# Kernel optimization log

Hardware: AMD Instinct MI355X
Metric: run time of the kernel (lower is better)

The kernel has to match this reference:

```python
import jax, jax.numpy as jnp
import numpy as np

B = 4096        # batch_size
D = 256         # feature_dim
N = 9000000     # dataset size (state buffer length)
G = 100         # num_groups
ALPHA = 0.5     # alpha_weight
GAMMA = 0.8
RHO = 8.0
LAM = 1.0       # lambada
ETA_P = 0.01
EPS = 1e-14
CLIP = 5.0


def setup_inputs() -> dict:
    key = jax.random.key(0)
    k = jax.random.split(key, 6)
    zis = jax.random.normal(k[0], (B, D), jnp.float32)
    zjs = jax.random.normal(k[1], (B, D), jnp.float32)
    # per-sample learned temperatures, small positive values
    taus_I = 0.01 + 0.2 * jax.random.uniform(k[2], (N,), jnp.float32)
    taus_T = 0.01 + 0.2 * jax.random.uniform(k[3], (N,), jnp.float32)
    group_info_I = jax.random.randint(k[4], (N,), 0, G, dtype=jnp.int32)
    group_info_T = jax.random.randint(k[5], (N,), 0, G, dtype=jnp.int32)
    ids = jnp.arange(B, dtype=jnp.int32)  # unique sample indices
    zeros_N = jnp.zeros((N,), jnp.float32)
    return {
        "zis": zis, "zjs": zjs,
        "s_I": zeros_N, "s_T": zeros_N, "b_I": zeros_N, "b_T": zeros_N,
        "z_I": jnp.zeros((G,), jnp.float32), "z_T": jnp.zeros((G,), jnp.float32),
        "p_I": jnp.ones((G,), jnp.float32) / G, "p_T": jnp.ones((G,), jnp.float32) / G,
        "taus_I": taus_I, "taus_T": taus_T,
        "ids": ids, "group_info_I": group_info_I, "group_info_T": group_info_T,
    }


def _l2norm(x):
    return x / jnp.maximum(jnp.linalg.norm(x, axis=1, keepdims=True), 1e-12)


def reference(zis, zjs, s_I, s_T, b_I, b_T, z_I, z_T, p_I, p_T,
              taus_I, taus_T, ids, group_info_I, group_info_T):
    zis = _l2norm(zis)
    zjs = _l2norm(zjs)
    sim = zis @ zjs.T                                   # [B, B]
    diag = jnp.diagonal(sim)                            # [B]
    mask_neg = 1.0 - jnp.eye(B, dtype=sim.dtype)
    image_diffs = sim - diag[:, None]
    text_diffs = sim - diag[None, :]

    tau_I = taus_I[ids]                                 # [B]
    tau_T = taus_T[ids]
    idt = jax.lax.stop_gradient(image_diffs / tau_I[:, None])
    tdt = jax.lax.stop_gradient(text_diffs / tau_T[None, :])

    # running max state (numerically-stable exp)
    old_b_I = b_I[ids]
    b_I_new = jnp.maximum(jnp.max(idt, axis=1), old_b_I)    # [B]
    old_b_T = b_T[ids]
    b_T_new = jnp.maximum(jnp.max(tdt, axis=0), old_b_T)    # [B]
    b_I = b_I.at[ids].set(b_I_new)
    b_T = b_T.at[ids].set(b_T_new)

    exp_I = jnp.exp(idt - b_I_new[:, None]) * mask_neg
    exp_T = jnp.exp(tdt - b_T_new[None, :]) * mask_neg
    g_I = jnp.sum(exp_I, axis=1)                         # [B]
    g_T = jnp.sum(exp_T, axis=0)                         # [B]

    # EMA of softmax denominators with max-rescaling
    s_I_new = (1.0 - GAMMA) * s_I[ids] * jnp.exp(old_b_I - b_I_new) + GAMMA * g_I
    s_T_new = (1.0 - GAMMA) * s_T[ids] * jnp.exp(old_b_T - b_T_new) + GAMMA * g_T
    s_I = s_I.at[ids].set(s_I_new)
    s_T = s_T.at[ids].set(s_T_new)
    s_I_c = jnp.maximum(s_I_new, EPS)
    s_T_c = jnp.maximum(s_T_new, EPS)

    w_I = exp_I / s_I_c[:, None]
    w_T = exp_T / s_T_c[None, :]

    gid_I = group_info_I[ids]                            # [B]
    gid_T = group_info_T[ids]
    gw_I = G * p_I[gid_I]                                # [B]
    gw_T = G * p_T[gid_T]

    image_loss = jnp.sum(w_I * gw_I[:, None] * image_diffs, axis=1)   # [B]
    text_loss = jnp.sum(w_T * gw_T[None, :] * text_diffs, axis=0)     # [B]
    total_loss = ALPHA * image_loss.mean() + (1.0 - ALPHA) * text_loss.mean()

    # per-group adversarial weight update
    F_I = tau_I * (jnp.log(s_I_c) + b_I_new + RHO)       # [B]
    F_T = tau_T * (jnp.log(s_T_c) + b_T_new + RHO)
    ones_b = jnp.ones((B,), sim.dtype)
    cnt_I = jnp.maximum(jax.ops.segment_sum(ones_b, gid_I, num_segments=G), 1.0)
    cnt_T = jnp.maximum(jax.ops.segment_sum(ones_b, gid_T, num_segments=G), 1.0)
    grad_p_I = jax.ops.segment_sum(F_I, gid_I, num_segments=G) / cnt_I
    grad_p_T = jax.ops.segment_sum(F_T, gid_T, num_segments=G) / cnt_T

    z_I = (1.0 - GAMMA) * z_I + GAMMA * grad_p_I
    z_T = (1.0 - GAMMA) * z_T + GAMMA * grad_p_T
    grad_hp_I = -LAM * jnp.log(p_I + EPS) - LAM
    grad_hp_T = -LAM * jnp.log(p_T + EPS) - LAM
    new_p_I = p_I * jnp.exp(2.0 * ETA_P * jnp.clip(z_I + grad_hp_I, -CLIP, CLIP))
    new_p_T = p_T * jnp.exp(2.0 * ETA_P * jnp.clip(z_T + grad_hp_T, -CLIP, CLIP))
    p_I = new_p_I / new_p_I.sum()
    p_T = new_p_T / new_p_T.sum()

    return total_loss, p_I, p_T
```

## Files before the change

### kernel.cpp

```cpp
#include <hip/hip_runtime.h>
#include <hip/hip_bf16.h>
#include <math.h>

#define BB 4096
#define DD 256
#define GG 100
#define GAMMA_C 0.8f
#define RHO_C 8.0f
#define ALPHA_C 0.5f
#define EPS_C 1e-14f
#define NSR 32
#define NSC 32

typedef __bf16 bf16x8 __attribute__((ext_vector_type(8)));
typedef float f32x16 __attribute__((ext_vector_type(16)));

__device__ inline float blockReduceSum(float v, float* lds) {
    for (int o = 32; o > 0; o >>= 1) v += __shfl_down(v, o);
    int lane = threadIdx.x & 63, wid = threadIdx.x >> 6;
    if (lane == 0) lds[wid] = v;
    __syncthreads();
    if (threadIdx.x == 0) {
        float r = lds[0];
        int nw = blockDim.x >> 6;
        for (int w = 1; w < nw; w++) r += lds[w];
        lds[0] = r;
    }
    __syncthreads();
    float r = lds[0];
    __syncthreads();
    return r;
}

__global__ void __launch_bounds__(256) norm_kernel(const float* __restrict__ zis,
                            const float* __restrict__ zjs,
                            ushort* __restrict__ zhi, ushort* __restrict__ zlo,
                            ushort* __restrict__ whi, ushort* __restrict__ wlo,
                            float* __restrict__ diag, float* __restrict__ acc) {
    __shared__ ushort st[4][4096];
    int rb = blockIdx.x;
    int wv = threadIdx.x >> 6, lane = threadIdx.x & 63;
    if (rb == 0) { acc[threadIdx.x] = 0.f; acc[threadIdx.x + 256] = 0.f; }
    for (int rr = 0; rr < 4; rr++) {
        int rloc = wv * 4 + rr;
        int r = rb * 16 + rloc;
        float4 zv = *(const float4*)&zis[r * DD + lane * 4];
        float4 wv4 = *(const float4*)&zjs[r * DD + lane * 4];
        float sz = zv.x * zv.x + zv.y * zv.y + zv.z * zv.z + zv.w * zv.w;
        float sw = wv4.x * wv4.x + wv4.y * wv4.y + wv4.z * wv4.z + wv4.w * wv4.w;
        float dt = zv.x * wv4.x + zv.y * wv4.y + zv.z * wv4.z + zv.w * wv4.w;
        for (int mask = 1; mask <= 32; mask <<= 1) {
            sz += __shfl_xor(sz, mask);
            sw += __shfl_xor(sw, mask);
            dt += __shfl_xor(dt, mask);
        }
        float iz = 1.0f / fmaxf(sqrtf(sz), 1e-12f);
        float iw = 1.0f / fmaxf(sqrtf(sw), 1e-12f);
        if (lane == 0) diag[r] = dt * iz * iw;
        float nz[4] = {zv.x * iz, zv.y * iz, zv.z * iz, zv.w * iz};
        float nw[4] = {wv4.x * iw, wv4.y * iw, wv4.z * iw, wv4.w * iw};
        for (int e = 0; e < 4; e++) {
            int k = lane * 4 + e;
            int li = ((k >> 4) << 8) | (((((k >> 3) & 1) << 4) | rloc) << 3) | (k & 7);
            __hip_bfloat16 hz = __float2bfloat16(nz[e]);
            __hip_bfloat16 lz = __float2bfloat16(nz[e] - __bfloat162float(hz));
            __hip_bfloat16 hw = __float2bfloat16(nw[e]);
            __hip_bfloat16 lw = __float2bfloat16(nw[e] - __bfloat162float(hw));
            st[0][li] = *(ushort*)&hz;
            st[1][li] = *(ushort*)&lz;
            st[2][li] = *(ushort*)&hw;
            st[3][li] = *(ushort*)&lw;
        }
    }
    __syncthreads();
    ushort* dsts[4] = {zhi, zlo, whi, wlo};
    int gbase = (rb >> 1) * 1024 + (rb & 1) * 16;
    for (int a = 0; a < 4; a++) {
        uint4* d = (uint4*)dsts[a];
        const uint4* s = (const uint4*)st[a];
        for (int it = 0; it < 2; it++) {
            int Lu = it * 256 + threadIdx.x;
            int Gu = gbase + (Lu >> 5) * 64 + ((Lu >> 4) & 1) * 32 + (Lu & 15);
            d[Gu] = s[Lu];
        }
    }
}

__global__ void __launch_bounds__(256, 4) fused_tile(const ushort* __restrict__ Ahi,
        const ushort* __restrict__ Alo, const ushort* __restrict__ Bhi,
        const ushort* __restrict__ Blo, const float* __restrict__ diag,
        const float* __restrict__ tausI, const float* __restrict__ tausT,
        const int* __restrict__ ids,
        float* __restrict__ pmR, float* __restrict__ pgR, float* __restrict__ pwR,
        float* __restrict__ pmC, float* __restrict__ pgC, float* __restrict__ pwC) {
    __shared__ float rDiag[128], rITau[128];
    __shared__ float cDiag[128], cITau[128];
    __shared__ float cmS[4][128], cgS[4][128], cwS[4][128];
    __shared__ float tr[4][32 * 65];

    int lane = threadIdx.x & 63;
    int wv = threadIdx.x >> 6;
    int bm = blockIdx.y * 128, bn = blockIdx.x * 128;
    int h = lane >> 5, cl = lane & 31;

    if (threadIdx.x < 128) {
        int r = bm + threadIdx.x;
        rDiag[threadIdx.x] = diag[r];
        rITau[threadIdx.x] = 1.0f / tausI[ids[r]];
    } else {
        int c = bn + threadIdx.x - 128;
        cDiag[threadIdx.x - 128] = diag[c];
        cITau[threadIdx.x - 128] = 1.0f / tausT[ids[c]];
    }

    int aBase = (blockIdx.y * 4 + wv) * 8192;
    int bB0 = (blockIdx.x * 4) * 8192;
    int lofs = lane * 8;

    f32x16 acc[4] = {};
#pragma unroll
    for (int s = 0; s < 16; s++) {
        int so = s * 512 + lofs;
        bf16x8 ah = *(const bf16x8*)&Ahi[aBase + so];
        bf16x8 al = *(const bf16x8*)&Alo[aBase + so];
        bf16x8 bh[4], bl[4];
#pragma unroll
        for (int j = 0; j < 4; j++) {
            bh[j] = *(const bf16x8*)&Bhi[bB0 + j * 8192 + so];
            bl[j] = *(const bf16x8*)&Blo[bB0 + j * 8192 + so];
        }
#pragma unroll
        for (int j = 0; j < 4; j++)
            acc[j] = __builtin_amdgcn_mfma_f32_32x32x16_bf16(ah, bh[j], acc[j], 0, 0, 0);
#pragma unroll
        for (int j = 0; j < 4; j++)
            acc[j] = __builtin_amdgcn_mfma_f32_32x32x16_bf16(ah, bl[j], acc[j], 0, 0, 0);
#pragma unroll
        for (int j = 0; j < 4; j++)
            acc[j] = __builtin_amdgcn_mfma_f32_32x32x16_bf16(al, bh[j], acc[j], 0, 0, 0);
    }

    __syncthreads();
#pragma unroll
    for (int u = 0; u < 4; u++) {
        int clc = u * 32 + cl;
        float cd = cDiag[clc];
        float cit = cITau[clc];
        float m = -INFINITY;
#pragma unroll
        for (int reg = 0; reg < 16; reg++) m = fmaxf(m, acc[u][reg]);
        m = fmaxf(m, __shfl_xor(m, 32));
        float cb = (m - cd) * cit;
        float cg = 0.f, cw = 0.f;
        int gc = bn + clc;
#pragma unroll
        for (int reg = 0; reg < 16; reg++) {
            int gr = bm + wv * 32 + (reg & 3) + 4 * h + 8 * (reg >> 2);
            float v = acc[u][reg];
            bool off = gr != gc;
            float dvT = v - cd;
            float eT = off ? __expf(dvT * cit - cb) : 0.f;
            cg += eT;
            cw += eT * dvT;
        }
        cg += __shfl_xor(cg, 32);
        cw += __shfl_xor(cw, 32);
        if (h == 0) {
            cmS[wv][clc] = cb;
            cgS[wv][clc] = cg;
            cwS[wv][clc] = cw;
        }
    }
    __syncthreads();

    if (threadIdx.x < 128) {
        int c = threadIdx.x;
        float m = fmaxf(fmaxf(cmS[0][c], cmS[1][c]), fmaxf(cmS[2][c], cmS[3][c]));
        float g = 0.f, w = 0.f;
        for (int wq = 0; wq < 4; wq++) {
            float f = __expf(cmS[wq][c] - m);
            g += cgS[wq][c] * f;
            w += cwS[wq][c] * f;
        }
        size_t o = (size_t)blockIdx.y * BB + bn + c;
        pmC[o] = m;
        pgC[o] = g;
        pwC[o] = w;
    }

    {
        int grow = bm + wv * 32 + cl;
        float rd = rDiag[wv * 32 + cl];
        float rit = rITau[wv * 32 + cl];
        float rm = -INFINITY, rg = 0.f, rw = 0.f;
#pragma unroll
        for (int ch = 0; ch < 2; ch++) {
#pragma unroll
            for (int uu = 0; uu < 2; uu++)
#pragma unroll
                for (int reg = 0; reg < 16; reg++) {
                    int r = (reg & 3) + 4 * h + 8 * (reg >> 2);
                    tr[wv][r * 65 + uu * 32 + cl] = acc[ch * 2 + uu][reg];
                }
            float vv[32];
#pragma unroll
            for (int j = 0; j < 32; j++) vv[j] = tr[wv][cl * 65 + h * 32 + j];
            float m0 = -INFINITY;
#pragma unroll
            for (int j = 0; j < 32; j++) m0 = fmaxf(m0, vv[j]);
            float g0 = 0.f, w0 = 0.f;
#pragma unroll
            for (int j = 0; j < 32; j++) {
                int gc = bn + ch * 64 + h * 32 + j;
                float dv = vv[j] - rd;
                float e = (grow != gc) ? __expf((vv[j] - m0) * rit) : 0.f;
                g0 += e;
                w0 += e * dv;
            }
            float mn = fmaxf(rm, m0);
            float fo = __expf((rm - mn) * rit);
            float fs = __expf((m0 - mn) * rit);
            rg = rg * fo + g0 * fs;
            rw = rw * fo + w0 * fs;
            rm = mn;
        }
        float mo = __shfl_xor(rm, 32);
        float go = __shfl_xor(rg, 32);
        float wo = __shfl_xor(rw, 32);
        float mn = fmaxf(rm, mo);
        rg = rg * __expf((rm - mn) * rit) + go * __expf((mo - mn) * rit);
        rw = rw * __expf((rm - mn) * rit) + wo * __expf((mo - mn) * rit);
        rm = mn;
        float bloc = (rm - rd) * rit;
        if (h == 0) {
            size_t o = (size_t)blockIdx.x * BB + grow;
            pmR[o] = bloc;
            pgR[o] = rg;
            pwR[o] = rw;
        }
    }
}

__global__ void __launch_bounds__(256) fin_kernel(
        const float* __restrict__ pmR, const float* __restrict__ pgR,
        const float* __restrict__ pwR, const float* __restrict__ pmC,
        const float* __restrict__ pgC, const float* __restrict__ pwC,
        const float* __restrict__ sI, const float* __restrict__ bI,
        const float* __restrict__ tausI, const int* __restrict__ gInfI,
        const float* __restrict__ pI,
        const float* __restrict__ sT, const float* __restrict__ bT,
        const float* __restrict__ tausT, const int* __restrict__ gInfT,
        const float* __restrict__ pT,
        const int* __restrict__ ids, float* __restrict__ acc,
        const float* __restrict__ zI, const float* __restrict__ zT,
        float* __restrict__ out) {
    __shared__ float lds[8];
    __shared__ float binF[GG], binC[GG];
    __shared__ float mS[8][32], gS[8][32], wS[8][32];
    __shared__ int lastFlag;
    if (threadIdx.x < GG) { binF[threadIdx.x] = 0.f; binC[threadIdx.x] = 0.f; }
    int side = blockIdx.x >> 7;
    int chunk = blockIdx.x & 127;
    int il = threadIdx.x & 31;
    int sg = threadIdx.x >> 5;
    int i = chunk * 32 + il;
    int ns = side ? NSC : NSR;
    const float* pm = side ? pmC : pmR;
    const float* pg = side ? pgC : pgR;
    const float* pw = side ? pwC : pwR;
    const float* sS = side ? sT : sI;
    const float* bS = side ? bT : bI;
    const float* taus = side ? tausT : tausI;
    const int* ginfo = side ? gInfT : gInfI;
    const float* pP = side ? pT : pI;

    float m = -INFINITY, g = 0.f, w = 0.f;
    for (int s = sg; s < ns; s += 8) {
        float pms = pm[(size_t)s * BB + i];
        float pgs = pg[(size_t)s * BB + i];
        float pws = pw[(size_t)s * BB + i];
        float mn = fmaxf(m, pms);
        float fo = __expf(m - mn);
        float fs = __expf(pms - mn);
        g = g * fo + pgs * fs;
        w = w * fo + pws * fs;
        m = mn;
    }
    mS[sg][il] = m;
    gS[sg][il] = g;
    wS[sg][il] = w;
    __syncthreads();

    float loss = 0.f;
    if (sg == 0) {
        int id = ids[i];
        float oldb = bS[id];
        float mm = mS[0][il];
        for (int q = 1; q < 8; q++) mm = fmaxf(mm, mS[q][il]);
        float bfin = fmaxf(mm, oldb);
        float gg2 = 0.f, ww2 = 0.f;
        for (int q = 0; q < 8; q++) {
            float f = __expf(mS[q][il] - bfin);
            gg2 += gS[q][il] * f;
            ww2 += wS[q][il] * f;
        }
        float tau = taus[id];
        float snew = (1.f - GAMMA_C) * sS[id] * expf(oldb - bfin) + GAMMA_C * gg2;
        float sc = fmaxf(snew, EPS_C);
        int gid = ginfo[id];
        float gw = (float)GG * pP[gid];
        loss = gw * ww2 / sc;
        float F = tau * (logf(sc) + bfin + RHO_C);
        atomicAdd(&binF[gid], F);
        atomicAdd(&binC[gid], 1.0f);
    }
    float lsum = blockReduceSum(loss, lds);
    if (threadIdx.x == 0) atomicAdd(&acc[side], lsum);
    __syncthreads();
    if (threadIdx.x < GG) {
        atomicAdd(&acc[2 + side * 200 + threadIdx.x], binF[threadIdx.x]);
        atomicAdd(&acc[102 + side * 200 + threadIdx.x], binC[threadIdx.x]);
    }

    __threadfence();
    if (threadIdx.x == 0) {
        int old = atomicAdd((int*)&acc[408], 1);
        lastFlag = (old == 255);
    }
    __syncthreads();
    if (!lastFlag) return;

    int gg = threadIdx.x;
    float npI = 0.f, npT = 0.f;
    if (gg < GG) {
        float cI = __hip_atomic_load(&acc[102 + gg], __ATOMIC_RELAXED, __HIP_MEMORY_SCOPE_AGENT);
        float fI = __hip_atomic_load(&acc[2 + gg], __ATOMIC_RELAXED, __HIP_MEMORY_SCOPE_AGENT);
        float gpI = fI / fmaxf(cI, 1.f);
        float zi = (1.f - GAMMA_C) * zI[gg] + GAMMA_C * gpI;
        float ghpI = -logf(pI[gg] + EPS_C) - 1.f;
        float ti = fminf(fmaxf(zi + ghpI, -5.f), 5.f);
        npI = pI[gg] * expf(0.02f * ti);

        float cT = __hip_atomic_load(&acc[302 + gg], __ATOMIC_RELAXED, __HIP_MEMORY_SCOPE_AGENT);
        float fT = __hip_atomic_load(&acc[202 + gg], __ATOMIC_RELAXED, __HIP_MEMORY_SCOPE_AGENT);
        float gpT = fT / fmaxf(cT, 1.f);
        float zt = (1.f - GAMMA_C) * zT[gg] + GAMMA_C * gpT;
        float ghpT = -logf(pT[gg] + EPS_C) - 1.f;
        float tt = fminf(fmaxf(zt + ghpT, -5.f), 5.f);
        npT = pT[gg] * expf(0.02f * tt);
    }
    float sumI = blockReduceSum(npI, lds);
    float sumT = blockReduceSum(npT, lds);
    if (gg < GG) {
        out[1 + gg] = npI / sumI;
        out[101 + gg] = npT / sumT;
    }
    if (gg == 0) {
        float lI = __hip_atomic_load(&acc[0], __ATOMIC_RELAXED, __HIP_MEMORY_SCOPE_AGENT);
        float lT = __hip_atomic_load(&acc[1], __ATOMIC_RELAXED, __HIP_MEMORY_SCOPE_AGENT);
        out[0] = ALPHA_C * (lI / (float)BB) + (1.f - ALPHA_C) * (lT / (float)BB);
    }
}

extern "C" void kernel_launch(void* const* d_in, const int* in_sizes, int n_in,
                              void* d_out, int out_size, void* d_ws, size_t ws_size,
                              hipStream_t stream) {
    const float* zis   = (const float*)d_in[0];
    const float* zjs   = (const float*)d_in[1];
    const float* s_I   = (const float*)d_in[2];
    const float* s_T   = (const float*)d_in[3];
    const float* b_I   = (const float*)d_in[4];
    const float* b_T   = (const float*)d_in[5];
    const float* z_I   = (const float*)d_in[6];
    const float* z_T   = (const float*)d_in[7];
    const float* p_I   = (const float*)d_in[8];
    const float* p_T   = (const float*)d_in[9];
    const float* tausI = (const float*)d_in[10];
    const float* tausT = (const float*)d_in[11];
    const int*   ids   = (const int*)d_in[12];
    const int*   gInfI = (const int*)d_in[13];
    const int*   gInfT = (const int*)d_in[14];
    float* out = (float*)d_out;

    char* ws = (char*)d_ws;
    ushort* zhi = (ushort*)ws;
    ushort* zlo = zhi + (size_t)BB * DD;
    ushort* whi = zlo + (size_t)BB * DD;
    ushort* wlo = whi + (size_t)BB * DD;
    float* acc  = (float*)(wlo + (size_t)BB * DD);
    float* diag = acc + 512;
    float* pmR  = diag + BB;
    float* pgR  = pmR + (size_t)NSR * BB;
    float* pwR  = pgR + (size_t)NSR * BB;
    float* pmC  = pwR + (size_t)NSR * BB;
    float* pgC  = pmC + (size_t)NSC * BB;
    float* pwC  = pgC + (size_t)NSC * BB;

    norm_kernel<<<256, 256, 0, stream>>>(zis, zjs, zhi, zlo, whi, wlo, diag, acc);
    fused_tile<<<dim3(32, 32), 256, 0, stream>>>(zhi, zlo, whi, wlo, diag,
            tausI, tausT, ids, pmR, pgR, pwR, pmC, pgC, pwC);
    fin_kernel<<<256, 256, 0, stream>>>(pmR, pgR, pwR, pmC, pgC, pwC,
            s_I, b_I, tausI, gInfI, p_I, s_T, b_T, tausT, gInfT, p_T, ids, acc,
            z_I, z_T, out);
}
```

Before: 271.8 us.

## Stage shared B tiles through double-buffered LDS instead of per-wave global loads

Each of the four waves used to load all eight B fragments (hi/lo times four column tiles) straight from global memory, so every wave in a block fetched the same data. Now each wave loads two of the eight B fragments per k-step into a double-buffered LDS pool, prefetching the next step while the MFMAs run, and all waves read B from LDS. The same pool is reused for the reduction scratch and the transpose buffer, which keeps LDS usage near its old level. The cost is a block-wide barrier every k-step and extra LDS traffic, which may hurt latency hiding at four blocks per CU.

```diff
diff --git a/kernel.cpp b/kernel.cpp
--- a/kernel.cpp
+++ b/kernel.cpp
@@ -86,6 +86,7 @@
     }
 }
 
+#define BSTG(p, st2, e) (((ushort*)pool)[((p) * 8 + (st2)) * 512 + (e)])
 __global__ void __launch_bounds__(256, 4) fused_tile(const ushort* __restrict__ Ahi,
         const ushort* __restrict__ Alo, const ushort* __restrict__ Bhi,
         const ushort* __restrict__ Blo, const float* __restrict__ diag,
@@ -95,8 +96,7 @@
         float* __restrict__ pmC, float* __restrict__ pgC, float* __restrict__ pwC) {
     __shared__ float rDiag[128], rITau[128];
     __shared__ float cDiag[128], cITau[128];
-    __shared__ float cmS[4][128], cgS[4][128], cwS[4][128];
-    __shared__ float tr[4][32 * 65];
+    __shared__ alignas(16) char pool[33280];
 
     int lane = threadIdx.x & 63;
     int wv = threadIdx.x >> 6;
@@ -117,17 +117,35 @@
     int bB0 = (blockIdx.x * 4) * 8192;
     int lofs = lane * 8;
 
+    int st0 = wv * 2;
+    const ushort* sgA = ((wv & 2) ? Blo : Bhi) + bB0 + (st0 & 3) * 8192;
+    const ushort* sgB = sgA + 8192;
+
+    {
+        uint4 p0 = *(const uint4*)(sgA + lofs);
+        uint4 p1 = *(const uint4*)(sgB + lofs);
+        *(uint4*)&BSTG(0, st0, lofs) = p0;
+        *(uint4*)&BSTG(0, st0 + 1, lofs) = p1;
+    }
+    __syncthreads();
+
     f32x16 acc[4] = {};
 #pragma unroll
     for (int s = 0; s < 16; s++) {
+        const int cur = s & 1;
+        uint4 sr0, sr1;
+        if (s < 15) {
+            sr0 = *(const uint4*)(sgA + (s + 1) * 512 + lofs);
+            sr1 = *(const uint4*)(sgB + (s + 1) * 512 + lofs);
+        }
         int so = s * 512 + lofs;
         bf16x8 ah = *(const bf16x8*)&Ahi[aBase + so];
         bf16x8 al = *(const bf16x8*)&Alo[aBase + so];
         bf16x8 bh[4], bl[4];
 #pragma unroll
         for (int j = 0; j < 4; j++) {
-            bh[j] = *(const bf16x8*)&Bhi[bB0 + j * 8192 + so];
-            bl[j] = *(const bf16x8*)&Blo[bB0 + j * 8192 + so];
+            bh[j] = *(const bf16x8*)&BSTG(cur, j, lofs);
+            bl[j] = *(const bf16x8*)&BSTG(cur, 4 + j, lofs);
         }
 #pragma unroll
         for (int j = 0; j < 4; j++)
@@ -138,9 +156,16 @@
 #pragma unroll
         for (int j = 0; j < 4; j++)
             acc[j] = __builtin_amdgcn_mfma_f32_32x32x16_bf16(al, bh[j], acc[j], 0, 0, 0);
-    }
-
-    __syncthreads();
+        if (s < 15) {
+            *(uint4*)&BSTG(cur ^ 1, st0, lofs) = sr0;
+            *(uint4*)&BSTG(cur ^ 1, st0 + 1, lofs) = sr1;
+        }
+        __syncthreads();
+    }
+
+    float* CM = (float*)pool;
+    float* CGp = CM + 512;
+    float* CWp = CM + 1024;
 #pragma unroll
     for (int u = 0; u < 4; u++) {
         int clc = u * 32 + cl;
@@ -166,29 +191,31 @@
         cg += __shfl_xor(cg, 32);
         cw += __shfl_xor(cw, 32);
         if (h == 0) {
-            cmS[wv][clc] = cb;
-            cgS[wv][clc] = cg;
-            cwS[wv][clc] = cw;
+            CM[wv * 128 + clc] = cb;
+            CGp[wv * 128 + clc] = cg;
+            CWp[wv * 128 + clc] = cw;
         }
     }
     __syncthreads();
 
     if (threadIdx.x < 128) {
         int c = threadIdx.x;
-        float m = fmaxf(fmaxf(cmS[0][c], cmS[1][c]), fmaxf(cmS[2][c], cmS[3][c]));
+        float m = fmaxf(fmaxf(CM[c], CM[128 + c]), fmaxf(CM[256 + c], CM[384 + c]));
         float g = 0.f, w = 0.f;
         for (int wq = 0; wq < 4; wq++) {
-            float f = __expf(cmS[wq][c] - m);
-            g += cgS[wq][c] * f;
-            w += cwS[wq][c] * f;
+            float f = __expf(CM[wq * 128 + c] - m);
+            g += CGp[wq * 128 + c] * f;
+            w += CWp[wq * 128 + c] * f;
         }
         size_t o = (size_t)blockIdx.y * BB + bn + c;
         pmC[o] = m;
         pgC[o] = g;
         pwC[o] = w;
     }
+    __syncthreads();
 
     {
+        float* trF = (float*)pool + wv * 2080;
         int grow = bm + wv * 32 + cl;
         float rd = rDiag[wv * 32 + cl];
         float rit = rITau[wv * 32 + cl];
@@ -200,11 +227,11 @@
 #pragma unroll
                 for (int reg = 0; reg < 16; reg++) {
                     int r = (reg & 3) + 4 * h + 8 * (reg >> 2);
-                    tr[wv][r * 65 + uu * 32 + cl] = acc[ch * 2 + uu][reg];
+                    trF[r * 65 + uu * 32 + cl] = acc[ch * 2 + uu][reg];
                 }
             float vv[32];
 #pragma unroll
-            for (int j = 0; j < 32; j++) vv[j] = tr[wv][cl * 65 + h * 32 + j];
+            for (int j = 0; j < 32; j++) vv[j] = trF[cl * 65 + h * 32 + j];
             float m0 = -INFINITY;
 #pragma unroll
             for (int j = 0; j < 32; j++) m0 = fmaxf(m0, vv[j]);
```

Result: no change. 269.3 us (-0.9%).
